# Performance work log

Measured on AMD Instinct MI355X. Metric: run time of the kernel, lower is better.

Reference implementation:

```python
import jax, jax.numpy as jnp
import numpy as np

B, S, D = 8, 2048, 1024
TEMPERATURE = 32.0  # sqrt(d_model)
NEG_INF = -1e16


def setup_inputs() -> dict:
    key = jax.random.key(0)
    ks = jax.random.split(key, 9)
    sc = 1.0 / np.sqrt(D)
    q = jax.random.normal(ks[0], (B, S, D), dtype=jnp.float32)
    k = jax.random.normal(ks[1], (B, S, D), dtype=jnp.float32)
    v = jax.random.normal(ks[2], (B, S, D), dtype=jnp.float32)
    # nn.Linear weights are [out, in]; init roughly uniform(-1/sqrt(in), 1/sqrt(in))
    Wq = jax.random.uniform(ks[3], (D, D), jnp.float32, -sc, sc)
    Wk = jax.random.uniform(ks[4], (D, D), jnp.float32, -sc, sc)
    Wv = jax.random.uniform(ks[5], (D, D), jnp.float32, -sc, sc)
    bq = jax.random.uniform(ks[6], (D,), jnp.float32, -sc, sc)
    bk = jax.random.uniform(ks[7], (D,), jnp.float32, -sc, sc)
    bv = jax.random.uniform(ks[8], (D,), jnp.float32, -sc, sc)
    # causal mask: True where attention is DISALLOWED (masked_fill semantics)
    mask = jnp.triu(jnp.ones((S, S), dtype=bool), k=1)
    mask = jnp.broadcast_to(mask[None, :, :], (B, S, S))
    return {"q": q, "k": k, "v": v, "Wq": Wq, "bq": bq, "Wk": Wk,
            "bk": bk, "Wv": Wv, "bv": bv, "mask": mask}


def reference(q, k, v, Wq, bq, Wk, bk, Wv, bv, mask):
    # Linear projections (torch Linear: x @ W.T + b)
    qp = jnp.einsum('bsd,ed->bse', q, Wq) + bq  # [B,S,D]
    kp = jnp.einsum('bsd,ed->bse', k, Wk) + bk
    vp = jnp.einsum('bsd,ed->bse', v, Wv) + bv
    # scores [B,S,S]
    attn = jnp.einsum('bsd,btd->bst', qp, kp) / TEMPERATURE
    attn = jnp.where(mask, NEG_INF, attn)
    attn = jax.nn.softmax(attn, axis=2)
    # dropout p=0.0 -> identity (eval mode)
    output = jnp.einsum('bst,btd->bsd', attn, vp)  # [B,S,D]
    return (output, attn)
```

## Files before the change

kernel.cpp:

```cpp
#include <hip/hip_runtime.h>
#include <hip/hip_bf16.h>
#include <stdint.h>

#define SEQ 2048
#define DIM 1024
#define NB  8

typedef __attribute__((ext_vector_type(8))) __bf16 bf16x8;
typedef __attribute__((ext_vector_type(8))) unsigned short ushort8;
typedef __attribute__((ext_vector_type(4))) float f32x4;

__device__ inline unsigned short f2b(float f) {
  union { float f; uint32_t u; } c; c.f = f;
  uint32_t u = c.u;
  return (unsigned short)((u + 0x7fffu + ((u >> 16) & 1u)) >> 16);
}

__device__ inline void async16(const void* g, void* l) {
  __builtin_amdgcn_global_load_lds((const __attribute__((address_space(1))) uint32_t*)g,
                                   (__attribute__((address_space(3))) uint32_t*)l,
                                   16, 0, 0);
}

__global__ __launch_bounds__(256) void cvt_f32_bf16(const float* __restrict__ in,
                                                    unsigned short* __restrict__ out, int n4) {
  int idx = blockIdx.x * 256 + threadIdx.x;
  int stride = gridDim.x * 256;
  for (int i = idx; i < n4; i += stride) {
    float4 f = ((const float4*)in)[i];
    ushort4 h;
    h.x = f2b(f.x); h.y = f2b(f.y); h.z = f2b(f.z); h.w = f2b(f.w);
    ((ushort4*)out)[i] = h;
  }
}

__device__ inline void remap_mn(int& bm, int& bn) {
  const int mT = gridDim.x, nT = gridDim.y;
  int did = blockIdx.y * mT + blockIdx.x;
  const int GM = 8;
  int per = GM * nT;
  int group = did / per;
  int rem = did - group * per;
  bm = group * GM + (rem % GM);
  bn = rem / GM;
}

template<int MODE>
__global__ __launch_bounds__(256)
void gemm_nt(const unsigned short* __restrict__ A,
             const unsigned short* __restrict__ B,
             void* __restrict__ Cv,
             const float* __restrict__ bias,
             int K, int lda, int ldb, int ldc,
             long long aStride, long long bStride, long long cStride,
             float scale)
{
  __shared__ __align__(16) unsigned short lA[2][128 * 32];
  __shared__ __align__(16) unsigned short lB[2][128 * 32];
  int bm, bn;
  remap_mn(bm, bn);
  if (MODE == 1 && bn > bm) return;
  const int bm0 = bm * 128;
  const int bn0 = bn * 128;
  const int z = blockIdx.z;
  A += (long long)z * aStride;
  B += (long long)z * bStride;
  const int tid  = threadIdx.x;
  const int lane = tid & 63;
  const int wv   = tid >> 6;
  const int wm   = (wv >> 1) * 64;
  const int wn   = (wv & 1) * 64;
  const int l15  = lane & 15;
  const int l4   = lane >> 4;
  const int Keff = (MODE == 2) ? (bm0 + 128) : K;

  f32x4 acc[4][4] = {};

  const int srow = tid >> 2;
  const int skb  = (tid & 3) * 16;
  const char* gA = (const char*)A + ((size_t)(bm0 + srow) * lda) * 2 + skb;
  const char* gB = (const char*)B + ((size_t)(bn0 + srow) * ldb) * 2 + skb;
  const size_t stepA = (size_t)64 * lda * 2;
  const size_t stepB = (size_t)64 * ldb * 2;

  auto stage = [&](int buf, int k0) {
    const char* ga = gA + (size_t)k0 * 2;
    const char* gb = gB + (size_t)k0 * 2;
    async16(ga,         &lA[buf][tid * 8]);
    async16(ga + stepA, &lA[buf][(tid + 256) * 8]);
    async16(gb,         &lB[buf][tid * 8]);
    async16(gb + stepB, &lB[buf][(tid + 256) * 8]);
  };

  stage(0, 0);
  int buf = 0;
  for (int k0 = 0; k0 < Keff; k0 += 32) {
    __syncthreads();
    if (k0 + 32 < Keff) stage(buf ^ 1, k0 + 32);
    bf16x8 af[4], bfr[4];
    #pragma unroll
    for (int i = 0; i < 4; ++i)
      af[i] = __builtin_bit_cast(bf16x8, *(const ushort8*)&lA[buf][(wm + i*16 + l15) * 32 + l4 * 8]);
    #pragma unroll
    for (int j = 0; j < 4; ++j)
      bfr[j] = __builtin_bit_cast(bf16x8, *(const ushort8*)&lB[buf][(wn + j*16 + l15) * 32 + l4 * 8]);
    #pragma unroll
    for (int i = 0; i < 4; ++i)
      #pragma unroll
      for (int j = 0; j < 4; ++j)
        acc[i][j] = __builtin_amdgcn_mfma_f32_16x16x32_bf16(af[i], bfr[j], acc[i][j], 0, 0, 0);
    buf ^= 1;
  }

  if (MODE == 0) {
    unsigned short* Ch = (unsigned short*)Cv;
    #pragma unroll
    for (int i = 0; i < 4; ++i)
      #pragma unroll
      for (int r = 0; r < 4; ++r) {
        int row = bm0 + wm + i * 16 + l4 * 4 + r;
        #pragma unroll
        for (int j = 0; j < 4; ++j) {
          int col = bn0 + wn + j * 16 + l15;
          Ch[(size_t)row * ldc + col] = f2b(acc[i][j][r] + bias[col]);
        }
      }
  } else {
    float* Cf = (float*)Cv + (long long)z * cStride;
    #pragma unroll
    for (int i = 0; i < 4; ++i)
      #pragma unroll
      for (int r = 0; r < 4; ++r) {
        int row = bm0 + wm + i * 16 + l4 * 4 + r;
        #pragma unroll
        for (int j = 0; j < 4; ++j) {
          int col = bn0 + wn + j * 16 + l15;
          Cf[(size_t)row * ldc + col] = acc[i][j][r] * scale;
        }
      }
  }
}

__global__ __launch_bounds__(256)
void softmax_causal(float* __restrict__ attnF, unsigned short* __restrict__ attnH) {
  const int S = SEQ;
  int row = blockIdx.x;
  int i = row & (S - 1);
  float* rp = attnF + (size_t)row * S;
  unsigned short* hp = attnH + (size_t)row * S;
  int len = i + 1;
  int tid = threadIdx.x;
  float vals[8];
  float m = -1e30f;
  #pragma unroll
  for (int it = 0; it < 8; ++it) {
    int j = it * 256 + tid;
    float v = (j < len) ? rp[j] : -1e30f;
    vals[it] = v;
    m = fmaxf(m, v);
  }
  #pragma unroll
  for (int o = 32; o > 0; o >>= 1) m = fmaxf(m, __shfl_xor(m, o, 64));
  __shared__ float red[4];
  int wv = tid >> 6, lane = tid & 63;
  if (lane == 0) red[wv] = m;
  __syncthreads();
  m = fmaxf(fmaxf(red[0], red[1]), fmaxf(red[2], red[3]));
  __syncthreads();
  float s = 0.f;
  #pragma unroll
  for (int it = 0; it < 8; ++it) {
    float e = __expf(vals[it] - m);
    vals[it] = e;
    s += e;
  }
  #pragma unroll
  for (int o = 32; o > 0; o >>= 1) s += __shfl_xor(s, o, 64);
  if (lane == 0) red[wv] = s;
  __syncthreads();
  s = red[0] + red[1] + red[2] + red[3];
  float inv = 1.f / s;
  #pragma unroll
  for (int it = 0; it < 8; ++it) {
    float o = vals[it] * inv;
    rp[it * 256 + tid] = o;
    hp[it * 256 + tid] = f2b(o);
  }
}

__global__ void transpose_bf16(const unsigned short* __restrict__ in, unsigned short* __restrict__ out) {
  __shared__ unsigned short tile[32][33];
  size_t zoff = (size_t)blockIdx.z * SEQ * DIM;
  const unsigned short* ip = in + zoff;
  unsigned short* op = out + zoff;
  int c0 = blockIdx.x * 32;
  int r0 = blockIdx.y * 32;
  int tx = threadIdx.x, ty = threadIdx.y;
  #pragma unroll
  for (int dy = 0; dy < 32; dy += 8)
    tile[ty + dy][tx] = ip[(size_t)(r0 + ty + dy) * DIM + c0 + tx];
  __syncthreads();
  #pragma unroll
  for (int dy = 0; dy < 32; dy += 8)
    op[(size_t)(c0 + ty + dy) * SEQ + r0 + tx] = tile[tx][ty + dy];
}

extern "C" void kernel_launch(void* const* d_in, const int* in_sizes, int n_in,
                              void* d_out, int out_size, void* d_ws, size_t ws_size,
                              hipStream_t stream) {
  (void)in_sizes; (void)n_in; (void)out_size; (void)ws_size;
  const int B = NB, S = SEQ, D = DIM;
  const size_t BSD = (size_t)B * S * D;
  const size_t BSS = (size_t)B * S * S;
  const size_t DD  = (size_t)D * D;

  const float* q  = (const float*)d_in[0];
  const float* k  = (const float*)d_in[1];
  const float* v  = (const float*)d_in[2];
  const float* Wq = (const float*)d_in[3];
  const float* bq = (const float*)d_in[4];
  const float* Wk = (const float*)d_in[5];
  const float* bk = (const float*)d_in[6];
  const float* Wv = (const float*)d_in[7];
  const float* bv = (const float*)d_in[8];

  float* out   = (float*)d_out;
  float* attnF = out + BSD;

  unsigned short* xb  = (unsigned short*)d_ws;
  unsigned short* Wqb = xb + BSD;
  unsigned short* Wkb = Wqb + DD;
  unsigned short* Wvb = Wkb + DD;
  unsigned short* qp  = Wvb + DD;
  unsigned short* kp  = qp + BSD;
  unsigned short* vp  = kp + BSD;
  unsigned short* attnH = vp;

  dim3 blk(256);
  cvt_f32_bf16<<<dim3(512), blk, 0, stream>>>(Wq, Wqb, (int)(DD / 4));
  cvt_f32_bf16<<<dim3(512), blk, 0, stream>>>(Wk, Wkb, (int)(DD / 4));
  cvt_f32_bf16<<<dim3(512), blk, 0, stream>>>(Wv, Wvb, (int)(DD / 4));
  cvt_f32_bf16<<<dim3(4096), blk, 0, stream>>>(q, xb, (int)(BSD / 4));
  gemm_nt<0><<<dim3(128, 8, 1), blk, 0, stream>>>(xb, Wqb, qp, bq, D, D, D, D, 0, 0, 0, 1.f);
  cvt_f32_bf16<<<dim3(4096), blk, 0, stream>>>(k, xb, (int)(BSD / 4));
  gemm_nt<0><<<dim3(128, 8, 1), blk, 0, stream>>>(xb, Wkb, kp, bk, D, D, D, D, 0, 0, 0, 1.f);
  cvt_f32_bf16<<<dim3(4096), blk, 0, stream>>>(v, xb, (int)(BSD / 4));
  gemm_nt<0><<<dim3(128, 8, 1), blk, 0, stream>>>(xb, Wvb, vp, bv, D, D, D, D, 0, 0, 0, 1.f);
  transpose_bf16<<<dim3(D / 32, S / 32, B), dim3(32, 8), 0, stream>>>(vp, xb);
  gemm_nt<1><<<dim3(S / 128, S / 128, B), blk, 0, stream>>>(qp, kp, attnF, nullptr,
      D, D, D, S, (long long)S * D, (long long)S * D, (long long)S * S, 1.f / 32.f);
  softmax_causal<<<dim3(B * S), blk, 0, stream>>>(attnF, attnH);
  gemm_nt<2><<<dim3(S / 128, D / 128, B), blk, 0, stream>>>(attnH, xb, out, nullptr,
      S, S, S, D, (long long)S * S, (long long)D * S, (long long)S * D, 1.f);
}
```

Measured before the change: 769.0 us.

## Replace GEMM with 256x256-tile, 8-wave kernel with swizzled LDS and explicit pipelining

The 128x128, 4-wave GEMM is replaced by a 256x256-tile kernel with 512 threads. It uses 128KB of dynamic LDS, double-buffered K=64 stages split into halves, and an XOR swizzle on LDS rows. Loads and MFMA phases are interleaved by hand using barriers, s_setprio, and explicit vmcnt/lgkmcnt waits. Tiles are remapped round-robin across XCD chunks. The goal is more data reuse per LDS byte and better overlap of loads with compute, at the cost of heavy LDS use that allows only one workgroup per CU, and coarser tiles for the causal-skip and triangular-K cases.

```diff
diff --git a/kernel.cpp b/kernel.cpp
--- a/kernel.cpp
+++ b/kernel.cpp
@@ -34,20 +34,9 @@
   }
 }
 
-__device__ inline void remap_mn(int& bm, int& bn) {
-  const int mT = gridDim.x, nT = gridDim.y;
-  int did = blockIdx.y * mT + blockIdx.x;
-  const int GM = 8;
-  int per = GM * nT;
-  int group = did / per;
-  int rem = did - group * per;
-  bm = group * GM + (rem % GM);
-  bn = rem / GM;
-}
-
 template<int MODE>
-__global__ __launch_bounds__(256)
-void gemm_nt(const unsigned short* __restrict__ A,
+__global__ __launch_bounds__(512, 2)
+void gemm256(const unsigned short* __restrict__ A,
              const unsigned short* __restrict__ B,
              void* __restrict__ Cv,
              const float* __restrict__ bias,
@@ -55,89 +44,184 @@
              long long aStride, long long bStride, long long cStride,
              float scale)
 {
-  __shared__ __align__(16) unsigned short lA[2][128 * 32];
-  __shared__ __align__(16) unsigned short lB[2][128 * 32];
-  int bm, bn;
-  remap_mn(bm, bn);
+  extern __shared__ __align__(16) unsigned short lds[];
+  unsigned short* const lA0 = lds;
+  unsigned short* const lB0 = lds + 4 * 8192;
+
+  const int mT = gridDim.x, nT = gridDim.y;
+  const int nwg = mT * nT;
+  const int did = blockIdx.y * mT + blockIdx.x;
+  const int chunk = nwg >> 3;
+  const int tile = (did & 7) * chunk + (did >> 3);
+  const int bm = tile / nT;
+  const int bn = tile % nT;
   if (MODE == 1 && bn > bm) return;
-  const int bm0 = bm * 128;
-  const int bn0 = bn * 128;
+  const int bm0 = bm << 8;
+  const int bn0 = bn << 8;
   const int z = blockIdx.z;
   A += (long long)z * aStride;
   B += (long long)z * bStride;
+
   const int tid  = threadIdx.x;
   const int lane = tid & 63;
   const int wv   = tid >> 6;
-  const int wm   = (wv >> 1) * 64;
-  const int wn   = (wv & 1) * 64;
+  const int wm   = wv >> 2;
+  const int wn   = wv & 3;
   const int l15  = lane & 15;
   const int l4   = lane >> 4;
-  const int Keff = (MODE == 2) ? (bm0 + 128) : K;
-
-  f32x4 acc[4][4] = {};
-
-  const int srow = tid >> 2;
-  const int skb  = (tid & 3) * 16;
-  const char* gA = (const char*)A + ((size_t)(bm0 + srow) * lda) * 2 + skb;
-  const char* gB = (const char*)B + ((size_t)(bn0 + srow) * ldb) * 2 + skb;
-  const size_t stepA = (size_t)64 * lda * 2;
-  const size_t stepB = (size_t)64 * ldb * 2;
-
-  auto stage = [&](int buf, int k0) {
-    const char* ga = gA + (size_t)k0 * 2;
-    const char* gb = gB + (size_t)k0 * 2;
-    async16(ga,         &lA[buf][tid * 8]);
-    async16(ga + stepA, &lA[buf][(tid + 256) * 8]);
-    async16(gb,         &lB[buf][tid * 8]);
-    async16(gb + stepB, &lB[buf][(tid + 256) * 8]);
+  const int Keff = (MODE == 2) ? (bm0 + 256) : K;
+  const int NT   = Keff >> 6;
+
+  auto LAh = [&](int buf, int kh) { return lA0 + ((buf << 1) + kh) * 8192; };
+  auto LBh = [&](int buf, int kh) { return lB0 + ((buf << 1) + kh) * 8192; };
+
+  const int rS   = tid >> 2;
+  const int cSrc = ((tid & 3) << 4) ^ ((rS & 3) << 4);
+  const char* gA0 = (const char*)A + ((size_t)(bm0 + rS) * lda) * 2 + cSrc;
+  const char* gA1 = gA0 + (size_t)128 * lda * 2;
+  const char* gB0 = (const char*)B + ((size_t)(bn0 + rS) * ldb) * 2 + cSrc;
+  const char* gB1 = gB0 + (size_t)128 * ldb * 2;
+
+  auto stageA = [&](int buf, int t64, int kh) {
+    size_t ko = (size_t)t64 * 128 + (size_t)(kh << 6);
+    unsigned short* d = LAh(buf, kh);
+    async16(gA0 + ko, d + tid * 8);
+    async16(gA1 + ko, d + (tid + 512) * 8);
   };
-
-  stage(0, 0);
-  int buf = 0;
-  for (int k0 = 0; k0 < Keff; k0 += 32) {
-    __syncthreads();
-    if (k0 + 32 < Keff) stage(buf ^ 1, k0 + 32);
-    bf16x8 af[4], bfr[4];
-    #pragma unroll
-    for (int i = 0; i < 4; ++i)
-      af[i] = __builtin_bit_cast(bf16x8, *(const ushort8*)&lA[buf][(wm + i*16 + l15) * 32 + l4 * 8]);
-    #pragma unroll
-    for (int j = 0; j < 4; ++j)
-      bfr[j] = __builtin_bit_cast(bf16x8, *(const ushort8*)&lB[buf][(wn + j*16 + l15) * 32 + l4 * 8]);
-    #pragma unroll
-    for (int i = 0; i < 4; ++i)
-      #pragma unroll
-      for (int j = 0; j < 4; ++j)
-        acc[i][j] = __builtin_amdgcn_mfma_f32_16x16x32_bf16(af[i], bfr[j], acc[i][j], 0, 0, 0);
-    buf ^= 1;
+  auto stageB = [&](int buf, int t64, int kh) {
+    size_t ko = (size_t)t64 * 128 + (size_t)(kh << 6);
+    unsigned short* d = LBh(buf, kh);
+    async16(gB0 + ko, d + tid * 8);
+    async16(gB1 + ko, d + (tid + 512) * 8);
+  };
+
+  const int swz = (l4 << 4) ^ ((l15 & 3) << 4);
+  int aOff[8], bOff[4];
+  #pragma unroll
+  for (int m = 0; m < 8; ++m) aOff[m] = ((wm << 7) + (m << 4) + l15) * 64 + swz;
+  #pragma unroll
+  for (int n = 0; n < 4; ++n) bOff[n] = ((wn << 6) + (n << 4) + l15) * 64 + swz;
+
+  auto rd = [&](const unsigned short* base, int off) -> bf16x8 {
+    return __builtin_bit_cast(bf16x8, *(const ushort8*)((const char*)base + off));
+  };
+
+  f32x4 acc[8][4] = {};
+  bf16x8 aF[8], bFa, bFb;
+
+  stageA(0, 0, 0); stageB(0, 0, 0); stageA(0, 0, 1); stageB(0, 0, 1);
+  stageA(1, 1, 0); stageB(1, 1, 0); stageA(1, 1, 1);
+  asm volatile("s_waitcnt vmcnt(6)" ::: "memory");
+  __builtin_amdgcn_s_barrier();
+  __builtin_amdgcn_sched_barrier(0);
+
+  for (int tt = 0; tt < NT; ++tt) {
+    const int buf = tt & 1;
+    const unsigned short* a0 = LAh(buf, 0);
+    const unsigned short* a1 = LAh(buf, 1);
+    const unsigned short* b0 = LBh(buf, 0);
+    const unsigned short* b1 = LBh(buf, 1);
+
+    #pragma unroll
+    for (int m = 0; m < 8; ++m) aF[m] = rd(a0, aOff[m]);
+    bFa = rd(b0, bOff[0]); bFb = rd(b0, bOff[1]);
+    if (tt + 1 < NT) stageB(buf ^ 1, tt + 1, 1);
+    __builtin_amdgcn_s_barrier();
+    asm volatile("s_waitcnt lgkmcnt(0)" ::: "memory");
+    __builtin_amdgcn_sched_barrier(0);
+    __builtin_amdgcn_s_setprio(1);
+    #pragma unroll
+    for (int m = 0; m < 8; ++m) {
+      acc[m][0] = __builtin_amdgcn_mfma_f32_16x16x32_bf16(aF[m], bFa, acc[m][0], 0, 0, 0);
+      acc[m][1] = __builtin_amdgcn_mfma_f32_16x16x32_bf16(aF[m], bFb, acc[m][1], 0, 0, 0);
+    }
+    __builtin_amdgcn_s_setprio(0);
+    __builtin_amdgcn_s_barrier();
+    __builtin_amdgcn_sched_barrier(0);
+
+    bFa = rd(b0, bOff[2]); bFb = rd(b0, bOff[3]);
+    if (tt + 2 < NT) stageA(buf, tt + 2, 0);
+    __builtin_amdgcn_s_barrier();
+    asm volatile("s_waitcnt lgkmcnt(0)" ::: "memory");
+    __builtin_amdgcn_sched_barrier(0);
+    __builtin_amdgcn_s_setprio(1);
+    #pragma unroll
+    for (int m = 0; m < 8; ++m) {
+      acc[m][2] = __builtin_amdgcn_mfma_f32_16x16x32_bf16(aF[m], bFa, acc[m][2], 0, 0, 0);
+      acc[m][3] = __builtin_amdgcn_mfma_f32_16x16x32_bf16(aF[m], bFb, acc[m][3], 0, 0, 0);
+    }
+    __builtin_amdgcn_s_setprio(0);
+    __builtin_amdgcn_s_barrier();
+    __builtin_amdgcn_sched_barrier(0);
+
+    #pragma unroll
+    for (int m = 0; m < 8; ++m) aF[m] = rd(a1, aOff[m]);
+    bFa = rd(b1, bOff[0]); bFb = rd(b1, bOff[1]);
+    if (tt + 2 < NT) stageB(buf, tt + 2, 0);
+    __builtin_amdgcn_s_barrier();
+    asm volatile("s_waitcnt lgkmcnt(0)" ::: "memory");
+    __builtin_amdgcn_sched_barrier(0);
+    __builtin_amdgcn_s_setprio(1);
+    #pragma unroll
+    for (int m = 0; m < 8; ++m) {
+      acc[m][0] = __builtin_amdgcn_mfma_f32_16x16x32_bf16(aF[m], bFa, acc[m][0], 0, 0, 0);
+      acc[m][1] = __builtin_amdgcn_mfma_f32_16x16x32_bf16(aF[m], bFb, acc[m][1], 0, 0, 0);
+    }
+    __builtin_amdgcn_s_setprio(0);
+    __builtin_amdgcn_s_barrier();
+    __builtin_amdgcn_sched_barrier(0);
+
+    bFa = rd(b1, bOff[2]); bFb = rd(b1, bOff[3]);
+    if (tt + 2 < NT) stageA(buf, tt + 2, 1);
+    __builtin_amdgcn_s_barrier();
+    asm volatile("s_waitcnt lgkmcnt(0)" ::: "memory");
+    __builtin_amdgcn_sched_barrier(0);
+    __builtin_amdgcn_s_setprio(1);
+    #pragma unroll
+    for (int m = 0; m < 8; ++m) {
+      acc[m][2] = __builtin_amdgcn_mfma_f32_16x16x32_bf16(aF[m], bFa, acc[m][2], 0, 0, 0);
+      acc[m][3] = __builtin_amdgcn_mfma_f32_16x16x32_bf16(aF[m], bFb, acc[m][3], 0, 0, 0);
+    }
+    __builtin_amdgcn_s_setprio(0);
+    if (tt + 2 < NT) asm volatile("s_waitcnt vmcnt(6)" ::: "memory");
+    else             asm volatile("s_waitcnt vmcnt(0)" ::: "memory");
+    __builtin_amdgcn_s_barrier();
+    __builtin_amdgcn_sched_barrier(0);
   }
 
   if (MODE == 0) {
     unsigned short* Ch = (unsigned short*)Cv;
-    #pragma unroll
-    for (int i = 0; i < 4; ++i)
+    float bvv[4];
+    #pragma unroll
+    for (int n = 0; n < 4; ++n) bvv[n] = bias[bn0 + (wn << 6) + (n << 4) + l15];
+    #pragma unroll
+    for (int m = 0; m < 8; ++m) {
+      int rowb = bm0 + (wm << 7) + (m << 4) + (l4 << 2);
       #pragma unroll
       for (int r = 0; r < 4; ++r) {
-        int row = bm0 + wm + i * 16 + l4 * 4 + r;
+        int row = rowb + r;
         #pragma unroll
-        for (int j = 0; j < 4; ++j) {
-          int col = bn0 + wn + j * 16 + l15;
-          Ch[(size_t)row * ldc + col] = f2b(acc[i][j][r] + bias[col]);
+        for (int n = 0; n < 4; ++n) {
+          int col = bn0 + (wn << 6) + (n << 4) + l15;
+          Ch[(size_t)row * ldc + col] = f2b(acc[m][n][r] + bvv[n]);
         }
       }
+    }
   } else {
     float* Cf = (float*)Cv + (long long)z * cStride;
     #pragma unroll
-    for (int i = 0; i < 4; ++i)
+    for (int m = 0; m < 8; ++m) {
+      int rowb = bm0 + (wm << 7) + (m << 4) + (l4 << 2);
       #pragma unroll
       for (int r = 0; r < 4; ++r) {
-        int row = bm0 + wm + i * 16 + l4 * 4 + r;
+        int row = rowb + r;
         #pragma unroll
-        for (int j = 0; j < 4; ++j) {
-          int col = bn0 + wn + j * 16 + l15;
-          Cf[(size_t)row * ldc + col] = acc[i][j][r] * scale;
+        for (int n = 0; n < 4; ++n) {
+          int col = bn0 + (wn << 6) + (n << 4) + l15;
+          Cf[(size_t)row * ldc + col] = acc[m][n][r] * scale;
         }
       }
+    }
   }
 }
 
@@ -211,7 +295,6 @@
   (void)in_sizes; (void)n_in; (void)out_size; (void)ws_size;
   const int B = NB, S = SEQ, D = DIM;
   const size_t BSD = (size_t)B * S * D;
-  const size_t BSS = (size_t)B * S * S;
   const size_t DD  = (size_t)D * D;
 
   const float* q  = (const float*)d_in[0];
@@ -236,20 +319,33 @@
   unsigned short* vp  = kp + BSD;
   unsigned short* attnH = vp;
 
+  static bool attrDone = []() {
+    hipFuncSetAttribute(reinterpret_cast<const void*>(&gemm256<0>),
+                        hipFuncAttributeMaxDynamicSharedMemorySize, 131072);
+    hipFuncSetAttribute(reinterpret_cast<const void*>(&gemm256<1>),
+                        hipFuncAttributeMaxDynamicSharedMemorySize, 131072);
+    hipFuncSetAttribute(reinterpret_cast<const void*>(&gemm256<2>),
+                        hipFuncAttributeMaxDynamicSharedMemorySize, 131072);
+    return true;
+  }();
+  (void)attrDone;
+
   dim3 blk(256);
+  dim3 gblk(512);
+  const size_t GLDS = 131072;
   cvt_f32_bf16<<<dim3(512), blk, 0, stream>>>(Wq, Wqb, (int)(DD / 4));
   cvt_f32_bf16<<<dim3(512), blk, 0, stream>>>(Wk, Wkb, (int)(DD / 4));
   cvt_f32_bf16<<<dim3(512), blk, 0, stream>>>(Wv, Wvb, (int)(DD / 4));
   cvt_f32_bf16<<<dim3(4096), blk, 0, stream>>>(q, xb, (int)(BSD / 4));
-  gemm_nt<0><<<dim3(128, 8, 1), blk, 0, stream>>>(xb, Wqb, qp, bq, D, D, D, D, 0, 0, 0, 1.f);
+  gemm256<0><<<dim3(64, 4, 1), gblk, GLDS, stream>>>(xb, Wqb, qp, bq, D, D, D, D, 0, 0, 0, 1.f);
   cvt_f32_bf16<<<dim3(4096), blk, 0, stream>>>(k, xb, (int)(BSD / 4));
-  gemm_nt<0><<<dim3(128, 8, 1), blk, 0, stream>>>(xb, Wkb, kp, bk, D, D, D, D, 0, 0, 0, 1.f);
+  gemm256<0><<<dim3(64, 4, 1), gblk, GLDS, stream>>>(xb, Wkb, kp, bk, D, D, D, D, 0, 0, 0, 1.f);
   cvt_f32_bf16<<<dim3(4096), blk, 0, stream>>>(v, xb, (int)(BSD / 4));
-  gemm_nt<0><<<dim3(128, 8, 1), blk, 0, stream>>>(xb, Wvb, vp, bv, D, D, D, D, 0, 0, 0, 1.f);
+  gemm256<0><<<dim3(64, 4, 1), gblk, GLDS, stream>>>(xb, Wvb, vp, bv, D, D, D, D, 0, 0, 0, 1.f);
   transpose_bf16<<<dim3(D / 32, S / 32, B), dim3(32, 8), 0, stream>>>(vp, xb);
-  gemm_nt<1><<<dim3(S / 128, S / 128, B), blk, 0, stream>>>(qp, kp, attnF, nullptr,
+  gemm256<1><<<dim3(S / 256, S / 256, B), gblk, GLDS, stream>>>(qp, kp, attnF, nullptr,
       D, D, D, S, (long long)S * D, (long long)S * D, (long long)S * S, 1.f / 32.f);
   softmax_causal<<<dim3(B * S), blk, 0, stream>>>(attnF, attnH);
-  gemm_nt<2><<<dim3(S / 128, D / 128, B), blk, 0, stream>>>(attnH, xb, out, nullptr,
+  gemm256<2><<<dim3(S / 256, D / 256, B), gblk, GLDS, stream>>>(attnH, xb, out, nullptr,
       S, S, S, D, (long long)S * S, (long long)D * S, (long long)S * D, 1.f);
 }
```

New measurement: 729.7 us. 5.1% less time.
